# Performance work log

Hardware: AMD Instinct MI355X
Metric: run time of the kernel (lower is better)

## Reference

```python
import jax, jax.numpy as jnp
import numpy as np


def setup_inputs() -> dict:
    key = jax.random.key(0)
    ks = jax.random.split(key, 8)
    B, C, H, W = 4, 256, 64, 64
    Cqk = C // 8
    s = 0.05
    return {
        "x": jax.random.normal(ks[0], (B, C, H, W), jnp.float32),
        "Wq": jax.random.normal(ks[1], (Cqk, C), jnp.float32) * s,
        "bq": jax.random.normal(ks[2], (Cqk,), jnp.float32) * s,
        "Wk": jax.random.normal(ks[3], (Cqk, C), jnp.float32) * s,
        "bk": jax.random.normal(ks[4], (Cqk,), jnp.float32) * s,
        "Wv": jax.random.normal(ks[5], (C, C), jnp.float32) * s,
        "bv": jax.random.normal(ks[6], (C,), jnp.float32) * s,
        "gamma": jax.random.normal(ks[7], (1,), jnp.float32),
    }


def reference(x, Wq, bq, Wk, bk, Wv, bv, gamma):
    B, C, H, W = x.shape
    N = H * W
    xf = x.reshape(B, C, N)                      # [B,C,N]
    # 1x1 convs == channel matmuls
    q = jnp.einsum('oc,bcn->bon', Wq, xf) + bq[None, :, None]   # [B,C/8,N]
    k = jnp.einsum('oc,bcn->bon', Wk, xf) + bk[None, :, None]   # [B,C/8,N]
    v = jnp.einsum('oc,bcn->bon', Wv, xf) + bv[None, :, None]   # [B,C,N]
    # scores[b,i,j] = <q[:,i], k[:,j]>; softmax over j (last dim)
    scores = jnp.einsum('bci,bcj->bij', q, k)                   # [B,N,N]
    attn = jax.nn.softmax(scores, axis=-1)
    # out[b,c,i] = sum_j v[b,c,j] * attn[b,i,j]
    out = jnp.einsum('bcj,bij->bci', v, attn).reshape(B, C, H, W)
    return gamma[0] * out + x
```

## Files before the change

### kernel.cpp

```cpp
#include <hip/hip_runtime.h>


#define B_ 4
#define C_ 256
#define N_ 4096
#define CQK 32
#define LOG2E 1.44269504088896340736f

typedef __attribute__((ext_vector_type(8))) short short8;
typedef __attribute__((ext_vector_type(4))) short short4v;
typedef __attribute__((ext_vector_type(4))) unsigned int uint4v;
typedef __attribute__((ext_vector_type(16))) float f32x16;
typedef __attribute__((ext_vector_type(4))) float f32x4;

__device__ __forceinline__ unsigned short f2bf(float f) {
  unsigned int u = __builtin_bit_cast(unsigned int, f);
  u = (u + 0x7fffu + ((u >> 16) & 1u)) >> 16;
  return (unsigned short)u;
}
__device__ __forceinline__ float bf2f(unsigned short s) {
  unsigned int u = ((unsigned int)s) << 16;
  return __builtin_bit_cast(float, u);
}
__device__ __forceinline__ short f32tof16(float f) {
  const _Float16 hf = (_Float16)f;
  return __builtin_bit_cast(short, hf);
}
__device__ __forceinline__ unsigned int cvtpk(float lo, float hi) {
  unsigned int r;
  asm("v_cvt_pk_bf16_f32 %0, %1, %2" : "=v"(r) : "v"(lo), "v"(hi));
  return r;
}
__device__ __forceinline__ f32x16 mfma16(short8 a, short8 b, f32x16 c) {
  return __builtin_amdgcn_mfma_f32_32x32x16_bf16(a, b, c, 0, 0, 0);
}
__device__ __forceinline__ int swz64(int row, int col) {
  return row * 64 + ((((col >> 3) ^ row) & 7) << 3) + (col & 7);
}

__global__ __launch_bounds__(256) void k_prep(
    const float* __restrict__ x, unsigned short* __restrict__ xthi,
    unsigned short* __restrict__ xtlo,
    const float* __restrict__ Wq, const float* __restrict__ Wk,
    const float* __restrict__ Wv,
    unsigned short* __restrict__ wqh, unsigned short* __restrict__ wql,
    unsigned short* __restrict__ wkh, unsigned short* __restrict__ wkl,
    unsigned short* __restrict__ wvh, unsigned short* __restrict__ wvl) {
  __shared__ __align__(16) float tile[64 * 65];
  const int bi = blockIdx.x;
  const int t = threadIdx.x;
  if (bi < 1024) {
    const int it = bi & 63, ct = (bi >> 6) & 3, b = bi >> 8;
    const int i0 = it * 64, c0 = ct * 64;
    {
      const int i = t & 63, cb = t >> 6;
#pragma unroll
      for (int z = 0; z < 16; ++z) {
        const int c = z * 4 + cb;
        tile[i * 65 + c] = x[(b * C_ + c0 + c) * N_ + i0 + i];
      }
    }
    __syncthreads();
    {
      const int ii = t >> 2, p = t & 3;
      short8 h0, h1, l0, l1;
#pragma unroll
      for (int e = 0; e < 16; ++e) {
        const float f = tile[ii * 65 + p * 16 + e];
        const unsigned short hb = f2bf(f);
        const unsigned short lb = f2bf(f - bf2f(hb));
        if (e < 8) { h0[e] = (short)hb; l0[e] = (short)lb; }
        else       { h1[e - 8] = (short)hb; l1[e - 8] = (short)lb; }
      }
      const int base = (b * N_ + i0 + ii) * C_ + c0 + p * 16;
      *(short8*)(xthi + base) = h0;
      *(short8*)(xthi + base + 8) = h1;
      *(short8*)(xtlo + base) = l0;
      *(short8*)(xtlo + base + 8) = l1;
    }
  } else {
    const int e = (bi - 1024) * 256 + t;
    const float* src; unsigned short *hi, *lo; int idx;
    if (e < 8192)        { src = Wq; hi = wqh; lo = wql; idx = e; }
    else if (e < 16384)  { src = Wk; hi = wkh; lo = wkl; idx = e - 8192; }
    else                 { src = Wv; hi = wvh; lo = wvl; idx = e - 16384; }
    float f = src[idx];
    if (e < 8192) f *= LOG2E;
    const unsigned short h = f2bf(f);
    hi[idx] = h;
    lo[idx] = f2bf(f - bf2f(h));
  }
}

__global__ __launch_bounds__(256) void k_proj(
    const unsigned short* __restrict__ wqh, const unsigned short* __restrict__ wql,
    const unsigned short* __restrict__ wkh, const unsigned short* __restrict__ wkl,
    const unsigned short* __restrict__ wvh, const unsigned short* __restrict__ wvl,
    const unsigned short* __restrict__ xthi, const unsigned short* __restrict__ xtlo,
    const float* __restrict__ bq, const float* __restrict__ bk,
    const float* __restrict__ bv,
    unsigned short* __restrict__ qhg, unsigned short* __restrict__ qlg,
    unsigned short* __restrict__ kfrh, unsigned short* __restrict__ kfrl,
    unsigned short* __restrict__ vfr) {
  __shared__ __align__(16) char sm[33792];
  unsigned short* awh = (unsigned short*)sm;
  unsigned short* awl = awh + 4096;
  unsigned short* bxh = awl + 4096;
  unsigned short* bxl = bxh + 4096;
  float* qt = (float*)sm;

  const int it = blockIdx.x, ot = blockIdx.y, b = blockIdx.z;
  const int i0 = it * 64, o0 = ot * 64;
  const int t = threadIdx.x, lane = t & 63, w = t >> 6, h = lane >> 5;
  const int mb = w >> 1, nb = w & 1;
  const int srow = t >> 2, sp = t & 3;

  const int og = o0 + srow;
  const unsigned short *wh, *wl;
  if (og < 32)      { wh = wqh + og * C_;        wl = wql + og * C_; }
  else if (og < 64) { wh = wkh + (og - 32) * C_; wl = wkl + (og - 32) * C_; }
  else              { wh = wvh + (og - 64) * C_; wl = wvl + (og - 64) * C_; }
  const unsigned short* xh = xthi + (b * N_ + i0 + srow) * C_;
  const unsigned short* xl = xtlo + (b * N_ + i0 + srow) * C_;

  f32x16 acc;
#pragma unroll
  for (int e = 0; e < 16; ++e) acc[e] = 0.f;
  const int m = 32 * mb + (lane & 31);
  const int n = 32 * nb + (lane & 31);

  for (int kt = 0; kt < 4; ++kt) {
    const int cb = kt * 64 + sp * 16;
    *(short8*)&awh[swz64(srow, sp * 16)]     = *(const short8*)(wh + cb);
    *(short8*)&awh[swz64(srow, sp * 16 + 8)] = *(const short8*)(wh + cb + 8);
    *(short8*)&awl[swz64(srow, sp * 16)]     = *(const short8*)(wl + cb);
    *(short8*)&awl[swz64(srow, sp * 16 + 8)] = *(const short8*)(wl + cb + 8);
    *(short8*)&bxh[swz64(srow, sp * 16)]     = *(const short8*)(xh + cb);
    *(short8*)&bxh[swz64(srow, sp * 16 + 8)] = *(const short8*)(xh + cb + 8);
    *(short8*)&bxl[swz64(srow, sp * 16)]     = *(const short8*)(xl + cb);
    *(short8*)&bxl[swz64(srow, sp * 16 + 8)] = *(const short8*)(xl + cb + 8);
    __syncthreads();
#pragma unroll
    for (int kk = 0; kk < 4; ++kk) {
      const int kb = kk * 16 + h * 8;
      const short8 ah  = *(const short8*)&awh[swz64(m, kb)];
      const short8 al2 = *(const short8*)&awl[swz64(m, kb)];
      const short8 bh  = *(const short8*)&bxh[swz64(n, kb)];
      const short8 bl2 = *(const short8*)&bxl[swz64(n, kb)];
      acc = mfma16(ah, bh, acc);
      acc = mfma16(ah, bl2, acc);
      acc = mfma16(al2, bh, acc);
    }
    __syncthreads();
  }

  if (ot > 0) {
    const int vbase = (b * 64 + it) * 16384 + (2 * (ot - 1) + mb) * 2048 +
                      (n >> 4) * 512 + 256 * ((n >> 3) & 1) + (n & 7);
#pragma unroll
    for (int e = 0; e < 16; ++e) {
      const int rr = (e & 3) + 8 * (e >> 2) + 4 * h;
      const int oc = o0 - 64 + 32 * mb + rr;
      vfr[vbase + rr * 8] = f2bf(acc[e] + bv[oc]);
    }
  } else {
#pragma unroll
    for (int e = 0; e < 16; ++e) {
      const int r = 32 * mb + (e & 3) + 8 * (e >> 2) + 4 * h;
      const float bias = (r < 32) ? bq[r] * LOG2E : bk[r - 32];
      qt[r * 65 + n] = acc[e] + bias;
    }
    __syncthreads();
    const int ii = t >> 2;
    short8 hv0, hv1, lv0, lv1;
#pragma unroll
    for (int e = 0; e < 16; ++e) {
      const float f = qt[(sp * 16 + e) * 65 + ii];
      const unsigned short hb = f2bf(f);
      const unsigned short lb = f2bf(f - bf2f(hb));
      if (e < 8) { hv0[e] = (short)hb; lv0[e] = (short)lb; }
      else       { hv1[e - 8] = (short)hb; lv1[e - 8] = (short)lb; }
    }
    if (sp < 2) {
      const int base = (b * N_ + i0 + ii) * CQK + sp * 16;
      *(short8*)(qhg + base) = hv0; *(short8*)(qhg + base + 8) = hv1;
      *(short8*)(qlg + base) = lv0; *(short8*)(qlg + base + 8) = lv1;
    } else {
      const int key = i0 + ii;
      const int j32t = key >> 5, jl = key & 31;
      const int kk = sp - 2;
      const size_t kb2 = ((size_t)(b * 128 + j32t) * 2 + kk) * 512;
      *(short8*)(kfrh + kb2 + jl * 8) = hv0;
      *(short8*)(kfrh + kb2 + (jl + 32) * 8) = hv1;
      *(short8*)(kfrl + kb2 + jl * 8) = lv0;
      *(short8*)(kfrl + kb2 + (jl + 32) * 8) = lv1;
    }
  }
}

__global__ __launch_bounds__(256, 2) void k_flash(
    const unsigned short* __restrict__ qhg, const unsigned short* __restrict__ qlg,
    const unsigned short* __restrict__ kfrh, const unsigned short* __restrict__ kfrl,
    const unsigned short* __restrict__ vfr,
    unsigned short* __restrict__ Opart, float* __restrict__ lpart) {
  const int blk = blockIdx.x;
  const int xs = blk & 7;
  const int b = xs >> 1;
  const int gl = blk >> 3;
  const int s = (xs & 1) * 2 + (gl & 1);
  const int t = threadIdx.x, lane = t & 63, w = t >> 6, h = lane >> 5;
  const int l31 = lane & 31;
  const int widx = (gl >> 1) * 4 + w;
  const int qw = widx >> 1, ch = widx & 1;
  const int srow = qw * 32 + l31;

  short8 qfh[2], qfl[2];
  {
    const unsigned short* qph = qhg + (size_t)(b * N_ + srow) * CQK + h * 8;
    const unsigned short* qpl = qlg + (size_t)(b * N_ + srow) * CQK + h * 8;
#pragma unroll
    for (int kk = 0; kk < 2; ++kk) {
      qfh[kk] = *(const short8*)(qph + kk * 16);
      qfl[kk] = *(const short8*)(qpl + kk * 16);
    }
  }
  const unsigned short* kbh = kfrh + (size_t)(b * 128 + s * 32) * 1024 + lane * 8;
  const unsigned short* kbl = kfrl + (size_t)(b * 128 + s * 32) * 1024 + lane * 8;
  short8 kfh[2][2], kfl[2][2];
  auto loadK = [&](int tau) {
#pragma unroll
    for (int jt = 0; jt < 2; ++jt)
#pragma unroll
      for (int kk = 0; kk < 2; ++kk) {
        const int off = ((tau * 2 + jt) * 2 + kk) * 512;
        kfh[jt][kk] = *(const short8*)(kbh + off);
        kfl[jt][kk] = *(const short8*)(kbl + off);
      }
  };
  loadK(0);
  const unsigned short* vbase =
      vfr + (size_t)(b * 64 + s * 16) * 16384 + (ch * 4) * 2048 + lane * 8;

  f32x16 acc0, acc1, acc2, acc3;
#pragma unroll
  for (int e = 0; e < 16; ++e) {
    acc0[e] = 0.f; acc1[e] = 0.f; acc2[e] = 0.f; acc3[e] = 0.f;
  }
  float l_run = 0.f;

  for (int kt = 0; kt < 16; ++kt) {
    __builtin_amdgcn_s_barrier();
    f32x16 s0, s1;
#pragma unroll
    for (int e = 0; e < 16; ++e) { s0[e] = 0.f; s1[e] = 0.f; }
    __builtin_amdgcn_s_setprio(1);
#pragma unroll
    for (int kk = 0; kk < 2; ++kk) {
      s0 = mfma16(kfh[0][kk], qfh[kk], s0);
      s0 = mfma16(kfh[0][kk], qfl[kk], s0);
      s0 = mfma16(kfl[0][kk], qfh[kk], s0);
      s1 = mfma16(kfh[1][kk], qfh[kk], s1);
      s1 = mfma16(kfh[1][kk], qfl[kk], s1);
      s1 = mfma16(kfl[1][kk], qfh[kk], s1);
    }
    __builtin_amdgcn_s_setprio(0);
    if (kt + 1 < 16) loadK(kt + 1);
#pragma unroll
    for (int e = 0; e < 16; ++e) s0[e] = __builtin_exp2f(s0[e]);
#pragma unroll
    for (int e = 0; e < 16; ++e) s1[e] = __builtin_exp2f(s1[e]);
    {
      float t8[8];
#pragma unroll
      for (int i2 = 0; i2 < 4; ++i2) {
        t8[i2] = (s0[4 * i2] + s0[4 * i2 + 1]) + (s0[4 * i2 + 2] + s0[4 * i2 + 3]);
        t8[4 + i2] = (s1[4 * i2] + s1[4 * i2 + 1]) + (s1[4 * i2 + 2] + s1[4 * i2 + 3]);
      }
      l_run += ((t8[0] + t8[1]) + (t8[2] + t8[3])) +
               ((t8[4] + t8[5]) + (t8[6] + t8[7]));
    }
    short8 pa0, pa1, pa2, pa3;
    {
      unsigned int w01 = cvtpk(s0[0], s0[1]),  w23 = cvtpk(s0[2], s0[3]);
      unsigned int w45 = cvtpk(s0[4], s0[5]),  w67 = cvtpk(s0[6], s0[7]);
      unsigned int w89 = cvtpk(s0[8], s0[9]),  wab = cvtpk(s0[10], s0[11]);
      unsigned int wcd = cvtpk(s0[12], s0[13]), wef = cvtpk(s0[14], s0[15]);
      unsigned int t01 = (unsigned)__shfl_xor((int)w01, 32);
      unsigned int t23 = (unsigned)__shfl_xor((int)w23, 32);
      unsigned int t45 = (unsigned)__shfl_xor((int)w45, 32);
      unsigned int t67 = (unsigned)__shfl_xor((int)w67, 32);
      unsigned int t89 = (unsigned)__shfl_xor((int)w89, 32);
      unsigned int tab = (unsigned)__shfl_xor((int)wab, 32);
      unsigned int tcd = (unsigned)__shfl_xor((int)wcd, 32);
      unsigned int tef = (unsigned)__shfl_xor((int)wef, 32);
      uint4v uA, uB;
      uA[0] = h ? t45 : w01;  uA[1] = h ? t67 : w23;
      uA[2] = h ? w45 : t01;  uA[3] = h ? w67 : t23;
      uB[0] = h ? tcd : w89;  uB[1] = h ? tef : wab;
      uB[2] = h ? wcd : t89;  uB[3] = h ? wef : tab;
      pa0 = __builtin_bit_cast(short8, uA);
      pa1 = __builtin_bit_cast(short8, uB);
    }
    {
      unsigned int w01 = cvtpk(s1[0], s1[1]),  w23 = cvtpk(s1[2], s1[3]);
      unsigned int w45 = cvtpk(s1[4], s1[5]),  w67 = cvtpk(s1[6], s1[7]);
      unsigned int w89 = cvtpk(s1[8], s1[9]),  wab = cvtpk(s1[10], s1[11]);
      unsigned int wcd = cvtpk(s1[12], s1[13]), wef = cvtpk(s1[14], s1[15]);
      unsigned int t01 = (unsigned)__shfl_xor((int)w01, 32);
      unsigned int t23 = (unsigned)__shfl_xor((int)w23, 32);
      unsigned int t45 = (unsigned)__shfl_xor((int)w45, 32);
      unsigned int t67 = (unsigned)__shfl_xor((int)w67, 32);
      unsigned int t89 = (unsigned)__shfl_xor((int)w89, 32);
      unsigned int tab = (unsigned)__shfl_xor((int)wab, 32);
      unsigned int tcd = (unsigned)__shfl_xor((int)wcd, 32);
      unsigned int tef = (unsigned)__shfl_xor((int)wef, 32);
      uint4v uA, uB;
      uA[0] = h ? t45 : w01;  uA[1] = h ? t67 : w23;
      uA[2] = h ? w45 : t01;  uA[3] = h ? w67 : t23;
      uB[0] = h ? tcd : w89;  uB[1] = h ? tef : wab;
      uB[2] = h ? wcd : t89;  uB[3] = h ? wef : tab;
      pa2 = __builtin_bit_cast(short8, uA);
      pa3 = __builtin_bit_cast(short8, uB);
    }
    {
      short8 vfA[4], vfB[4];
#pragma unroll
      for (int sl = 0; sl < 4; ++sl) {
        vfA[sl] = *(const short8*)(vbase + kt * 16384 + 0 * 2048 + sl * 512);
        vfB[sl] = *(const short8*)(vbase + kt * 16384 + 1 * 2048 + sl * 512);
      }
      __builtin_amdgcn_s_setprio(1);
      acc0 = mfma16(pa0, vfA[0], acc0);
      acc0 = mfma16(pa1, vfA[1], acc0);
      acc0 = mfma16(pa2, vfA[2], acc0);
      acc0 = mfma16(pa3, vfA[3], acc0);
      acc1 = mfma16(pa0, vfB[0], acc1);
      acc1 = mfma16(pa1, vfB[1], acc1);
      acc1 = mfma16(pa2, vfB[2], acc1);
      acc1 = mfma16(pa3, vfB[3], acc1);
      __builtin_amdgcn_s_setprio(0);
    }
    {
      short8 vfA[4], vfB[4];
#pragma unroll
      for (int sl = 0; sl < 4; ++sl) {
        vfA[sl] = *(const short8*)(vbase + kt * 16384 + 2 * 2048 + sl * 512);
        vfB[sl] = *(const short8*)(vbase + kt * 16384 + 3 * 2048 + sl * 512);
      }
      __builtin_amdgcn_s_setprio(1);
      acc2 = mfma16(pa0, vfA[0], acc2);
      acc2 = mfma16(pa1, vfA[1], acc2);
      acc2 = mfma16(pa2, vfA[2], acc2);
      acc2 = mfma16(pa3, vfA[3], acc2);
      acc3 = mfma16(pa0, vfB[0], acc3);
      acc3 = mfma16(pa1, vfB[1], acc3);
      acc3 = mfma16(pa2, vfB[2], acc3);
      acc3 = mfma16(pa3, vfB[3], acc3);
      __builtin_amdgcn_s_setprio(0);
    }
  }

  const float lfull = l_run + __shfl_xor(l_run, 32);
  if (ch == 0 && h == 0) {
    lpart[(size_t)(s * 4 + b) * 4096 + srow] = lfull;
  }
  const float invo = 1.0f / lfull;
  float invr[16];
#pragma unroll
  for (int e = 0; e < 16; ++e)
    invr[e] = __shfl(invo, (e & 3) + 8 * (e >> 2) + 4 * h);
  {
    const int wv = ((s * 4 + b) * 128 + qw) * 2 + ch;
    unsigned short* dst = Opart + (size_t)wv * 4096 + lane * 8;
    short8 o;
#pragma unroll
    for (int e = 0; e < 8; ++e) o[e] = f32tof16(acc0[e] * invr[e]);
    *(short8*)(dst + 0 * 512) = o;
#pragma unroll
    for (int e = 0; e < 8; ++e) o[e] = f32tof16(acc0[8 + e] * invr[8 + e]);
    *(short8*)(dst + 1 * 512) = o;
#pragma unroll
    for (int e = 0; e < 8; ++e) o[e] = f32tof16(acc1[e] * invr[e]);
    *(short8*)(dst + 2 * 512) = o;
#pragma unroll
    for (int e = 0; e < 8; ++e) o[e] = f32tof16(acc1[8 + e] * invr[8 + e]);
    *(short8*)(dst + 3 * 512) = o;
#pragma unroll
    for (int e = 0; e < 8; ++e) o[e] = f32tof16(acc2[e] * invr[e]);
    *(short8*)(dst + 4 * 512) = o;
#pragma unroll
    for (int e = 0; e < 8; ++e) o[e] = f32tof16(acc2[8 + e] * invr[8 + e]);
    *(short8*)(dst + 5 * 512) = o;
#pragma unroll
    for (int e = 0; e < 8; ++e) o[e] = f32tof16(acc3[e] * invr[e]);
    *(short8*)(dst + 6 * 512) = o;
#pragma unroll
    for (int e = 0; e < 8; ++e) o[e] = f32tof16(acc3[8 + e] * invr[8 + e]);
    *(short8*)(dst + 7 * 512) = o;
  }
}

__global__ __launch_bounds__(256) void k_combine(
    const unsigned short* __restrict__ Opart, const float* __restrict__ lpart,
    const float* __restrict__ x, const float* __restrict__ gamma,
    float* __restrict__ out) {
  const int cb = blockIdx.x;
  const int b = cb & 3, qt_ = cb >> 2;
  const int q0 = qt_ * 64;
  const int t = threadIdx.x;
  const int i = t & 63, cg = t >> 6;
  const int qg = q0 + i;

  float lv[4];
#pragma unroll
  for (int s = 0; s < 4; ++s) lv[s] = lpart[(size_t)(s * 4 + b) * 4096 + qg];
  const float L = (lv[0] + lv[1]) + (lv[2] + lv[3]);
  const float giv = gamma[0] / L;
  float sc[4];
#pragma unroll
  for (int s = 0; s < 4; ++s) sc[s] = lv[s] * giv;

  const int qw = qg >> 5, qi = qg & 31;
  const int h = (qi >> 2) & 1;
  const int hi8 = qi >> 4;
  const int eo = (qi & 3) + 4 * ((qi >> 3) & 1);
#pragma unroll 4
  for (int c = cg; c < C_; c += 4) {
    const int ch = c >> 7, ct = (c >> 5) & 3, ln = (c & 31) + 32 * h;
    const size_t sub = (size_t)(ct * 2 + hi8) * 512 + ln * 8 + eo;
    float acc = 0.f;
#pragma unroll
    for (int s = 0; s < 4; ++s) {
      const size_t o =
          (size_t)(((s * 4 + b) * 128 + qw) * 2 + ch) * 4096 + sub;
      acc += sc[s] * (float)__builtin_bit_cast(_Float16, Opart[o]);
    }
    const int g = (b * C_ + c) * N_ + qg;
    out[g] = acc + x[g];
  }
}

extern "C" void kernel_launch(void* const* d_in, const int* in_sizes, int n_in,
                              void* d_out, int out_size, void* d_ws, size_t ws_size,
                              hipStream_t stream) {
  const float* x     = (const float*)d_in[0];
  const float* Wq    = (const float*)d_in[1];
  const float* bq    = (const float*)d_in[2];
  const float* Wk    = (const float*)d_in[3];
  const float* bk    = (const float*)d_in[4];
  const float* Wv    = (const float*)d_in[5];
  const float* bv    = (const float*)d_in[6];
  const float* gamma = (const float*)d_in[7];
  float* out = (float*)d_out;
  (void)in_sizes; (void)n_in; (void)out_size; (void)ws_size;

  char* ws = (char*)d_ws;
  size_t off = 0;
  auto carve = [&](size_t bytes) -> char* {
    char* p = ws + off;
    off += (bytes + 255) & ~(size_t)255;
    return p;
  };
  unsigned short* xthi = (unsigned short*)carve((size_t)B_ * N_ * C_ * 2);
  unsigned short* xtlo = (unsigned short*)carve((size_t)B_ * N_ * C_ * 2);
  unsigned short* wqh  = (unsigned short*)carve(32 * 256 * 2);
  unsigned short* wql  = (unsigned short*)carve(32 * 256 * 2);
  unsigned short* wkh  = (unsigned short*)carve(32 * 256 * 2);
  unsigned short* wkl  = (unsigned short*)carve(32 * 256 * 2);
  unsigned short* wvh  = (unsigned short*)carve(256 * 256 * 2);
  unsigned short* wvl  = (unsigned short*)carve(256 * 256 * 2);
  unsigned short* qhg  = (unsigned short*)carve((size_t)B_ * N_ * CQK * 2);
  unsigned short* qlg  = (unsigned short*)carve((size_t)B_ * N_ * CQK * 2);
  unsigned short* kfrh = (unsigned short*)carve((size_t)B_ * N_ * CQK * 2);
  unsigned short* kfrl = (unsigned short*)carve((size_t)B_ * N_ * CQK * 2);
  unsigned short* vfr  = (unsigned short*)carve((size_t)B_ * C_ * N_ * 2);
  unsigned short* Opart = (unsigned short*)carve((size_t)4096 * 4096 * 2);
  float* lpart = (float*)carve((size_t)16 * 4096 * 4);

  k_prep<<<1344, 256, 0, stream>>>(x, xthi, xtlo, Wq, Wk, Wv,
                                   wqh, wql, wkh, wkl, wvh, wvl);
  k_proj<<<dim3(64, 5, B_), 256, 0, stream>>>(wqh, wql, wkh, wkl, wvh, wvl,
                                              xthi, xtlo, bq, bk, bv,
                                              qhg, qlg, kfrh, kfrl, vfr);
  k_flash<<<1024, 256, 0, stream>>>(qhg, qlg, kfrh, kfrl, vfr, Opart, lpart);
  k_combine<<<256, 256, 0, stream>>>(Opart, lpart, x, gamma, out);
}
```

Baseline: 188.1 us.

## Split score tiles across wave pairs and exchange probabilities via LDS

Before this change, the two waves sharing a query row block (ch=0/1) each computed the full 64-key score tile, its exp, and its bf16 packing. Each wave of the pair now handles only its own 32-key half. It writes the packed probabilities and partial row sums to shared memory, waits on a barrier, and reads the partner's half to build the full P fragments for the PV MFMAs. This halves the QK MFMA and exp work and the K register loads. The cost is an extra LDS round trip and a second block-wide barrier per key tile.

```diff
diff --git a/kernel.cpp b/kernel.cpp
--- a/kernel.cpp
+++ b/kernel.cpp
@@ -37,6 +37,8 @@
 __device__ __forceinline__ int swz64(int row, int col) {
   return row * 64 + ((((col >> 3) ^ row) & 7) << 3) + (col & 7);
 }
+
+#define WAITCNT(s) asm volatile("s_waitcnt " s ::: "memory")
 
 __global__ __launch_bounds__(256) void k_prep(
     const float* __restrict__ x, unsigned short* __restrict__ xthi,
@@ -203,6 +205,8 @@
     const unsigned short* __restrict__ kfrh, const unsigned short* __restrict__ kfrl,
     const unsigned short* __restrict__ vfr,
     unsigned short* __restrict__ Opart, float* __restrict__ lpart) {
+  __shared__ __align__(16) char sm[9216];
+
   const int blk = blockIdx.x;
   const int xs = blk & 7;
   const int b = xs >> 1;
@@ -214,6 +218,11 @@
   const int qw = widx >> 1, ch = widx & 1;
   const int srow = qw * 32 + l31;
 
+  unsigned int* paown = (unsigned int*)sm + w * 512 + lane;
+  unsigned int* papar = (unsigned int*)sm + (w ^ 1) * 512 + lane;
+  float* tsown = (float*)(sm + 8192) + w * 64 + lane;
+  float* tspar = (float*)(sm + 8192) + (w ^ 1) * 64 + lane;
+
   short8 qfh[2], qfl[2];
   {
     const unsigned short* qph = qhg + (size_t)(b * N_ + srow) * CQK + h * 8;
@@ -226,16 +235,14 @@
   }
   const unsigned short* kbh = kfrh + (size_t)(b * 128 + s * 32) * 1024 + lane * 8;
   const unsigned short* kbl = kfrl + (size_t)(b * 128 + s * 32) * 1024 + lane * 8;
-  short8 kfh[2][2], kfl[2][2];
+  short8 kfh[2], kfl[2];
   auto loadK = [&](int tau) {
 #pragma unroll
-    for (int jt = 0; jt < 2; ++jt)
-#pragma unroll
-      for (int kk = 0; kk < 2; ++kk) {
-        const int off = ((tau * 2 + jt) * 2 + kk) * 512;
-        kfh[jt][kk] = *(const short8*)(kbh + off);
-        kfl[jt][kk] = *(const short8*)(kbl + off);
-      }
+    for (int kk = 0; kk < 2; ++kk) {
+      const int off = ((tau * 2 + ch) * 2 + kk) * 512;
+      kfh[kk] = *(const short8*)(kbh + off);
+      kfl[kk] = *(const short8*)(kbl + off);
+    }
   };
   loadK(0);
   const unsigned short* vbase =
@@ -249,42 +256,36 @@
   float l_run = 0.f;
 
   for (int kt = 0; kt < 16; ++kt) {
+    WAITCNT("lgkmcnt(0)");
     __builtin_amdgcn_s_barrier();
-    f32x16 s0, s1;
-#pragma unroll
-    for (int e = 0; e < 16; ++e) { s0[e] = 0.f; s1[e] = 0.f; }
+    f32x16 sS;
+#pragma unroll
+    for (int e = 0; e < 16; ++e) sS[e] = 0.f;
     __builtin_amdgcn_s_setprio(1);
 #pragma unroll
     for (int kk = 0; kk < 2; ++kk) {
-      s0 = mfma16(kfh[0][kk], qfh[kk], s0);
-      s0 = mfma16(kfh[0][kk], qfl[kk], s0);
-      s0 = mfma16(kfl[0][kk], qfh[kk], s0);
-      s1 = mfma16(kfh[1][kk], qfh[kk], s1);
-      s1 = mfma16(kfh[1][kk], qfl[kk], s1);
-      s1 = mfma16(kfl[1][kk], qfh[kk], s1);
+      sS = mfma16(kfh[kk], qfh[kk], sS);
+      sS = mfma16(kfh[kk], qfl[kk], sS);
+      sS = mfma16(kfl[kk], qfh[kk], sS);
     }
     __builtin_amdgcn_s_setprio(0);
     if (kt + 1 < 16) loadK(kt + 1);
 #pragma unroll
-    for (int e = 0; e < 16; ++e) s0[e] = __builtin_exp2f(s0[e]);
-#pragma unroll
-    for (int e = 0; e < 16; ++e) s1[e] = __builtin_exp2f(s1[e]);
-    {
-      float t8[8];
-#pragma unroll
-      for (int i2 = 0; i2 < 4; ++i2) {
-        t8[i2] = (s0[4 * i2] + s0[4 * i2 + 1]) + (s0[4 * i2 + 2] + s0[4 * i2 + 3]);
-        t8[4 + i2] = (s1[4 * i2] + s1[4 * i2 + 1]) + (s1[4 * i2 + 2] + s1[4 * i2 + 3]);
-      }
-      l_run += ((t8[0] + t8[1]) + (t8[2] + t8[3])) +
-               ((t8[4] + t8[5]) + (t8[6] + t8[7]));
-    }
-    short8 pa0, pa1, pa2, pa3;
-    {
-      unsigned int w01 = cvtpk(s0[0], s0[1]),  w23 = cvtpk(s0[2], s0[3]);
-      unsigned int w45 = cvtpk(s0[4], s0[5]),  w67 = cvtpk(s0[6], s0[7]);
-      unsigned int w89 = cvtpk(s0[8], s0[9]),  wab = cvtpk(s0[10], s0[11]);
-      unsigned int wcd = cvtpk(s0[12], s0[13]), wef = cvtpk(s0[14], s0[15]);
+    for (int e = 0; e < 16; ++e) sS[e] = __builtin_exp2f(sS[e]);
+    float ts;
+    {
+      float t4[4];
+#pragma unroll
+      for (int i2 = 0; i2 < 4; ++i2)
+        t4[i2] = (sS[4 * i2] + sS[4 * i2 + 1]) + (sS[4 * i2 + 2] + sS[4 * i2 + 3]);
+      ts = (t4[0] + t4[1]) + (t4[2] + t4[3]);
+    }
+    unsigned int u0, u1, u2, u3, u4, u5, u6, u7;
+    {
+      unsigned int w01 = cvtpk(sS[0], sS[1]),  w23 = cvtpk(sS[2], sS[3]);
+      unsigned int w45 = cvtpk(sS[4], sS[5]),  w67 = cvtpk(sS[6], sS[7]);
+      unsigned int w89 = cvtpk(sS[8], sS[9]),  wab = cvtpk(sS[10], sS[11]);
+      unsigned int wcd = cvtpk(sS[12], sS[13]), wef = cvtpk(sS[14], sS[15]);
       unsigned int t01 = (unsigned)__shfl_xor((int)w01, 32);
       unsigned int t23 = (unsigned)__shfl_xor((int)w23, 32);
       unsigned int t45 = (unsigned)__shfl_xor((int)w45, 32);
@@ -293,34 +294,31 @@
       unsigned int tab = (unsigned)__shfl_xor((int)wab, 32);
       unsigned int tcd = (unsigned)__shfl_xor((int)wcd, 32);
       unsigned int tef = (unsigned)__shfl_xor((int)wef, 32);
-      uint4v uA, uB;
-      uA[0] = h ? t45 : w01;  uA[1] = h ? t67 : w23;
-      uA[2] = h ? w45 : t01;  uA[3] = h ? w67 : t23;
-      uB[0] = h ? tcd : w89;  uB[1] = h ? tef : wab;
-      uB[2] = h ? wcd : t89;  uB[3] = h ? wef : tab;
-      pa0 = __builtin_bit_cast(short8, uA);
-      pa1 = __builtin_bit_cast(short8, uB);
-    }
-    {
-      unsigned int w01 = cvtpk(s1[0], s1[1]),  w23 = cvtpk(s1[2], s1[3]);
-      unsigned int w45 = cvtpk(s1[4], s1[5]),  w67 = cvtpk(s1[6], s1[7]);
-      unsigned int w89 = cvtpk(s1[8], s1[9]),  wab = cvtpk(s1[10], s1[11]);
-      unsigned int wcd = cvtpk(s1[12], s1[13]), wef = cvtpk(s1[14], s1[15]);
-      unsigned int t01 = (unsigned)__shfl_xor((int)w01, 32);
-      unsigned int t23 = (unsigned)__shfl_xor((int)w23, 32);
-      unsigned int t45 = (unsigned)__shfl_xor((int)w45, 32);
-      unsigned int t67 = (unsigned)__shfl_xor((int)w67, 32);
-      unsigned int t89 = (unsigned)__shfl_xor((int)w89, 32);
-      unsigned int tab = (unsigned)__shfl_xor((int)wab, 32);
-      unsigned int tcd = (unsigned)__shfl_xor((int)wcd, 32);
-      unsigned int tef = (unsigned)__shfl_xor((int)wef, 32);
-      uint4v uA, uB;
-      uA[0] = h ? t45 : w01;  uA[1] = h ? t67 : w23;
-      uA[2] = h ? w45 : t01;  uA[3] = h ? w67 : t23;
-      uB[0] = h ? tcd : w89;  uB[1] = h ? tef : wab;
-      uB[2] = h ? wcd : t89;  uB[3] = h ? wef : tab;
-      pa2 = __builtin_bit_cast(short8, uA);
-      pa3 = __builtin_bit_cast(short8, uB);
+      u0 = h ? t45 : w01;  u1 = h ? t67 : w23;
+      u2 = h ? w45 : t01;  u3 = h ? w67 : t23;
+      u4 = h ? tcd : w89;  u5 = h ? tef : wab;
+      u6 = h ? wcd : t89;  u7 = h ? wef : tab;
+    }
+    paown[0 * 64] = u0;  paown[1 * 64] = u1;
+    paown[2 * 64] = u2;  paown[3 * 64] = u3;
+    paown[4 * 64] = u4;  paown[5 * 64] = u5;
+    paown[6 * 64] = u6;  paown[7 * 64] = u7;
+    *tsown = ts;
+    WAITCNT("lgkmcnt(0)");
+    __builtin_amdgcn_s_barrier();
+    unsigned int p0 = papar[0 * 64], p1 = papar[1 * 64];
+    unsigned int p2 = papar[2 * 64], p3 = papar[3 * 64];
+    unsigned int p4 = papar[4 * 64], p5 = papar[5 * 64];
+    unsigned int p6 = papar[6 * 64], p7 = papar[7 * 64];
+    l_run += ts + *tspar;
+    short8 jf0, jf1, jf2, jf3;
+    {
+      uint4v A0 = {u0, u1, u2, u3}, A1 = {u4, u5, u6, u7};
+      uint4v P0 = {p0, p1, p2, p3}, P1 = {p4, p5, p6, p7};
+      jf0 = __builtin_bit_cast(short8, ch ? P0 : A0);
+      jf1 = __builtin_bit_cast(short8, ch ? P1 : A1);
+      jf2 = __builtin_bit_cast(short8, ch ? A0 : P0);
+      jf3 = __builtin_bit_cast(short8, ch ? A1 : P1);
     }
     {
       short8 vfA[4], vfB[4];
@@ -330,14 +328,14 @@
         vfB[sl] = *(const short8*)(vbase + kt * 16384 + 1 * 2048 + sl * 512);
       }
       __builtin_amdgcn_s_setprio(1);
-      acc0 = mfma16(pa0, vfA[0], acc0);
-      acc0 = mfma16(pa1, vfA[1], acc0);
-      acc0 = mfma16(pa2, vfA[2], acc0);
-      acc0 = mfma16(pa3, vfA[3], acc0);
-      acc1 = mfma16(pa0, vfB[0], acc1);
-      acc1 = mfma16(pa1, vfB[1], acc1);
-      acc1 = mfma16(pa2, vfB[2], acc1);
-      acc1 = mfma16(pa3, vfB[3], acc1);
+      acc0 = mfma16(jf0, vfA[0], acc0);
+      acc0 = mfma16(jf1, vfA[1], acc0);
+      acc0 = mfma16(jf2, vfA[2], acc0);
+      acc0 = mfma16(jf3, vfA[3], acc0);
+      acc1 = mfma16(jf0, vfB[0], acc1);
+      acc1 = mfma16(jf1, vfB[1], acc1);
+      acc1 = mfma16(jf2, vfB[2], acc1);
+      acc1 = mfma16(jf3, vfB[3], acc1);
       __builtin_amdgcn_s_setprio(0);
     }
     {
@@ -348,14 +346,14 @@
         vfB[sl] = *(const short8*)(vbase + kt * 16384 + 3 * 2048 + sl * 512);
       }
       __builtin_amdgcn_s_setprio(1);
-      acc2 = mfma16(pa0, vfA[0], acc2);
-      acc2 = mfma16(pa1, vfA[1], acc2);
-      acc2 = mfma16(pa2, vfA[2], acc2);
-      acc2 = mfma16(pa3, vfA[3], acc2);
-      acc3 = mfma16(pa0, vfB[0], acc3);
-      acc3 = mfma16(pa1, vfB[1], acc3);
-      acc3 = mfma16(pa2, vfB[2], acc3);
-      acc3 = mfma16(pa3, vfB[3], acc3);
+      acc2 = mfma16(jf0, vfA[0], acc2);
+      acc2 = mfma16(jf1, vfA[1], acc2);
+      acc2 = mfma16(jf2, vfA[2], acc2);
+      acc2 = mfma16(jf3, vfA[3], acc2);
+      acc3 = mfma16(jf0, vfB[0], acc3);
+      acc3 = mfma16(jf1, vfB[1], acc3);
+      acc3 = mfma16(jf2, vfB[2], acc3);
+      acc3 = mfma16(jf3, vfB[3], acc3);
       __builtin_amdgcn_s_setprio(0);
     }
   }
```

New measurement: 175.8 us. 6.5% less time.
